# Optimization experiments

Hardware: AMD Instinct MI355X
Metric: run time of the kernel (lower is better)

Reference implementation:

```python
import jax, jax.numpy as jnp
import numpy as np

D_MAIN = 256
D_HID = 512  # int(d_main * d_multiplier)
N_NUM = 96
B = 1024
N_CAND = 100000
LN_EPS = 1e-5


def _ln(x, g, b):
    mu = x.mean(-1, keepdims=True)
    var = ((x - mu) ** 2).mean(-1, keepdims=True)
    return (x - mu) / jnp.sqrt(var + LN_EPS) * g + b


def _block(x, W1, b1, W2, b2):
    # Linear -> ReLU -> (Dropout=id) -> Linear -> (Dropout=id), residual added by caller
    return jnp.maximum(x @ W1 + b1, 0.0) @ W2 + b2


def setup_inputs() -> dict:
    key = jax.random.key(0)
    ks = jax.random.split(key, 32)

    def w(i, shape):
        fan_in = shape[0]
        return jax.random.normal(ks[i], shape, jnp.float32) / np.sqrt(fan_in)

    return {
        "x_num": jax.random.normal(ks[0], (B, N_NUM), jnp.float32),
        "cand_x_num": jax.random.normal(ks[1], (N_CAND, N_NUM), jnp.float32),
        "cand_y": jax.random.normal(ks[2], (N_CAND, 1), jnp.float32),
        "context_size": 96,
        # input linear
        "W_in": w(3, (N_NUM, D_MAIN)), "b_in": jnp.zeros((D_MAIN,), jnp.float32),
        # encoder block (no norm: first block)
        "We1": w(4, (D_MAIN, D_HID)), "be1": jnp.zeros((D_HID,), jnp.float32),
        "We2": w(5, (D_HID, D_MAIN)), "be2": jnp.zeros((D_MAIN,), jnp.float32),
        # mixer LayerNorm (mixer_normalization='auto' with encoder_n_blocks>0)
        "g_m": jnp.ones((D_MAIN,), jnp.float32), "b_m": jnp.zeros((D_MAIN,), jnp.float32),
        # S: key projection
        "Ws": w(6, (D_MAIN, D_MAIN)), "bs": jnp.zeros((D_MAIN,), jnp.float32),
        "Wy": w(7, (1, D_MAIN)), "by": jnp.zeros((D_MAIN,), jnp.float32),
        # V_t: Linear(no bias) -> ReLU -> Linear
        "Wt1": w(8, (D_MAIN, D_HID)),
        "Wt2": w(9, (D_HID, D_MAIN)), "bt2": jnp.zeros((D_MAIN,), jnp.float32),
        # predictor block (no norm: first block)
        "Wp1": w(10, (D_MAIN, D_HID)), "bp1": jnp.zeros((D_HID,), jnp.float32),
        "Wp2": w(11, (D_HID, D_MAIN)), "bp2": jnp.zeros((D_MAIN,), jnp.float32),
        # head P: LayerNorm -> ReLU -> Linear(d_main, 1)
        "g_h": jnp.ones((D_MAIN,), jnp.float32), "b_h": jnp.zeros((D_MAIN,), jnp.float32),
        "Wh": w(12, (D_MAIN, 1)), "bh": jnp.zeros((1,), jnp.float32),
    }


def _encode(x, W_in, b_in, We1, be1, We2, be2, g_m, b_m, Ws, bs):
    h = x @ W_in + b_in
    h = h + _block(h, We1, be1, We2, be2)
    k = _ln(h, g_m, b_m) @ Ws + bs
    return h, k


def reference(x_num, cand_x_num, cand_y, context_size,
              W_in, b_in, We1, be1, We2, be2, g_m, b_m, Ws, bs,
              Wy, by, Wt1, Wt2, bt2, Wp1, bp1, Wp2, bp2, g_h, b_h, Wh, bh):
    # encode queries and candidates with shared weights
    x, k = _encode(x_num, W_in, b_in, We1, be1, We2, be2, g_m, b_m, Ws, bs)
    _, ck = _encode(cand_x_num, W_in, b_in, We1, be1, We2, be2, g_m, b_m, Ws, bs)

    # similarities = -||k - ck||^2  [B, N_CAND]
    sim = (2.0 * (k @ ck.T)
           - (k * k).sum(-1, keepdims=True)
           - (ck * ck).sum(-1)[None, :])

    top_sim, idx = jax.lax.top_k(sim, context_size)   # [B, m]
    probs = jax.nn.softmax(top_sim, axis=-1)           # context_dropout = id in eval

    ctx_k = ck[idx]                                    # [B, m, d_main]
    ctx_y = cand_y[idx]                                # [B, m, 1]

    # values = V_y(y) + V_t(k - ctx_k)
    v = (ctx_y @ Wy + by
         + jnp.maximum((k[:, None, :] - ctx_k) @ Wt1, 0.0) @ Wt2 + bt2)

    x = x + jnp.einsum('bm,bmd->bd', probs, v)

    # predictor block + head
    x = x + _block(x, Wp1, bp1, Wp2, bp2)
    out = jnp.maximum(_ln(x, g_h, b_h), 0.0) @ Wh + bh  # [B, 1]
    return out
```

## Files before the change

### kernel.cpp

```cpp
#include <hip/hip_runtime.h>
#include <stdint.h>

#define NCAND 100000
#define NB    1024
#define DNUM  96
#define DM    256
#define DH    512
#define MCTX  96
#define LNEPS 1e-5f

typedef __bf16 bf16x8 __attribute__((ext_vector_type(8)));
typedef float  f32x4  __attribute__((ext_vector_type(4)));
typedef unsigned short u16x8 __attribute__((ext_vector_type(8)));
typedef unsigned short us;

__device__ __forceinline__ us f2bf(float x)
{
    unsigned u = __float_as_uint(x);
    unsigned r = u + 0x7FFFu + ((u >> 16) & 1u);
    return (us)(r >> 16);
}
__device__ __forceinline__ float bfbits(us h)
{
    return __uint_as_float(((unsigned)h) << 16);
}

extern "C" __global__ __launch_bounds__(256)
void split_k(const float* X, us* Xh, us* Xl, long long n)
{
    long long i = (long long)blockIdx.x * 256 + threadIdx.x;
    if (i < n) {
        float x = X[i];
        us h = f2bf(x);
        Xh[i] = h;
        Xl[i] = f2bf(x - bfbits(h));
    }
}

extern "C" __global__ __launch_bounds__(256)
void packW_k(const float* W, us* Ph, us* Pl, int Kd, int Nd)
{
    int i = blockIdx.x * 256 + threadIdx.x;
    if (i >= Kd * Nd) return;
    int e = i & 7, lane = (i >> 3) & 63, r = i >> 9;
    int KT = Kd >> 5;
    int kt = r % KT, jt = r / KT;
    int n = jt * 16 + (lane & 15);
    int k = kt * 32 + (lane >> 4) * 8 + e;
    float x = W[(long long)k * Nd + n];
    us h = f2bf(x);
    Ph[i] = h;
    Pl[i] = f2bf(x - bfbits(h));
}

extern "C" __global__ __launch_bounds__(256)
void packR_k(const us* Rh, const us* Rl, us* Ph, us* Pl, int Kd, int total)
{
    int i = blockIdx.x * 256 + threadIdx.x;
    if (i >= total) return;
    int e = i & 7, lane = (i >> 3) & 63, r = i >> 9;
    int KT = Kd >> 5;
    int kt = r % KT, jt = r / KT;
    int n = jt * 16 + (lane & 15);
    int k = kt * 32 + (lane >> 4) * 8 + e;
    Ph[i] = Rh[(long long)n * Kd + k];
    Pl[i] = Rl[(long long)n * Kd + k];
}

extern "C" __global__ __launch_bounds__(256)
void gemm_d(const us* Ah, const us* Al, const us* BPh, const us* BPl,
            float* outF, us* outH, us* outL, us* outB16,
            const float* bias, const us* Rh, const us* Rl, int dorelu,
            const float* lng, const float* lnb, us* lnH, us* lnL,
            float* snOut,
            const us* Gqh, const us* Gql, const us* Gch, const us* Gcl,
            const int* gidx,
            float* simT, const float* colb,
            int M, int N, int K)
{
    __shared__ float red1[256];
    __shared__ float red2[256];
    __shared__ float mu_s[64];
    __shared__ float rs_s[64];
    int t = threadIdx.x, wave = t >> 6, lane = t & 63;
    int lm = lane & 15, lk = (lane >> 4) * 8, rb = (lane >> 4) * 4;
    int m0b = blockIdx.x * 64;
    int n0 = blockIdx.y * 256;
    int KT = K >> 5;
    int jt0 = (n0 >> 4) + wave * 4;

    f32x4 acc[4][4];
#pragma unroll
    for (int i = 0; i < 4; i++)
#pragma unroll
        for (int j = 0; j < 4; j++)
            for (int e = 0; e < 4; e++) acc[i][j][e] = 0.0f;

    int gb4[4], gc4[4];
    if (gidx) {
#pragma unroll
        for (int i = 0; i < 4; i++) {
            int grow = m0b + i * 16 + lm;
            if (grow < M) { gb4[i] = grow / MCTX; gc4[i] = gidx[grow]; }
            else          { gb4[i] = 0; gc4[i] = 0; }
        }
    }

    for (int kt = 0; kt < KT; kt++) {
        int k0 = kt * 32;
        bf16x8 fah[4], fal[4];
#pragma unroll
        for (int i = 0; i < 4; i++) {
            int arow = m0b + i * 16 + lm;
            u16x8 ah8 = {0,0,0,0,0,0,0,0}, al8 = ah8;
            if (arow < M) {
                if (!gidx) {
                    ah8 = *(const u16x8*)(Ah + (long long)arow * K + k0 + lk);
                    al8 = *(const u16x8*)(Al + (long long)arow * K + k0 + lk);
                } else {
                    u16x8 qh = *(const u16x8*)(Gqh + (long long)gb4[i] * DM + k0 + lk);
                    u16x8 ql = *(const u16x8*)(Gql + (long long)gb4[i] * DM + k0 + lk);
                    u16x8 ch = *(const u16x8*)(Gch + (long long)gc4[i] * DM + k0 + lk);
                    u16x8 cl = *(const u16x8*)(Gcl + (long long)gc4[i] * DM + k0 + lk);
#pragma unroll
                    for (int e = 0; e < 8; e++) {
                        float v = (bfbits(qh[e]) + bfbits(ql[e]))
                                - (bfbits(ch[e]) + bfbits(cl[e]));
                        ah8[e] = f2bf(v);
                    }
                }
            }
            fah[i] = *(bf16x8*)&ah8;
            fal[i] = *(bf16x8*)&al8;
        }
#pragma unroll
        for (int j = 0; j < 4; j++) {
            long long bo = ((long long)(jt0 + j) * KT + kt) * 512 + lane * 8;
            u16x8 bu  = *(const u16x8*)(BPh + bo);
            u16x8 blu = *(const u16x8*)(BPl + bo);
            bf16x8 fbh = *(bf16x8*)&bu;
            bf16x8 fbl = *(bf16x8*)&blu;
#pragma unroll
            for (int i = 0; i < 4; i++) {
                acc[i][j] = __builtin_amdgcn_mfma_f32_16x16x32_bf16(fah[i], fbh, acc[i][j], 0, 0, 0);
                acc[i][j] = __builtin_amdgcn_mfma_f32_16x16x32_bf16(fah[i], fbl, acc[i][j], 0, 0, 0);
                if (!gidx)
                    acc[i][j] = __builtin_amdgcn_mfma_f32_16x16x32_bf16(fal[i], fbh, acc[i][j], 0, 0, 0);
            }
        }
    }

    if (simT) {
#pragma unroll
        for (int i = 0; i < 4; i++) {
            int cb = m0b + i * 16;
            if (cb >= M) break;
#pragma unroll
            for (int j = 0; j < 4; j++) {
                int q = n0 + wave * 64 + j * 16 + lm;
                f32x4 v;
                for (int e = 0; e < 4; e++)
                    v[e] = 2.0f * acc[i][j][e] - colb[cb + rb + e];
                *(f32x4*)(simT + (long long)q * NCAND + cb + rb) = v;
            }
        }
        return;
    }

#pragma unroll
    for (int j = 0; j < 4; j++) {
        int col = n0 + wave * 64 + j * 16 + lm;
        float bc = bias ? bias[col] : 0.0f;
#pragma unroll
        for (int i = 0; i < 4; i++) {
            for (int e = 0; e < 4; e++) {
                int row = m0b + i * 16 + rb + e;
                float v = acc[i][j][e] + bc;
                if (row < M) {
                    long long oix = (long long)row * N + col;
                    if (Rh) v += bfbits(Rh[oix]) + bfbits(Rl[oix]);
                    if (dorelu && v < 0.0f) v = 0.0f;
                    if (outF)   outF[oix] = v;
                    if (outB16) outB16[oix] = f2bf(v);
                    if (outH) { us h = f2bf(v); outH[oix] = h; outL[oix] = f2bf(v - bfbits(h)); }
                } else {
                    if (dorelu && v < 0.0f) v = 0.0f;
                }
                acc[i][j][e] = v;
            }
        }
    }

    if (lng || snOut) {
#pragma unroll
        for (int i = 0; i < 4; i++) {
            for (int e = 0; e < 4; e++) {
                int lr = i * 16 + rb + e;
                float s1 = 0.0f, s2 = 0.0f;
#pragma unroll
                for (int j = 0; j < 4; j++) { float v = acc[i][j][e]; s1 += v; s2 += v * v; }
                for (int o = 1; o < 16; o <<= 1) {
                    s1 += __shfl_xor(s1, o, 64);
                    s2 += __shfl_xor(s2, o, 64);
                }
                if (lm == 0) { red1[lr * 4 + wave] = s1; red2[lr * 4 + wave] = s2; }
            }
        }
        __syncthreads();
        if (t < 64) {
            float a = red1[t*4] + red1[t*4+1] + red1[t*4+2] + red1[t*4+3];
            float b2 = red2[t*4] + red2[t*4+1] + red2[t*4+2] + red2[t*4+3];
            if (lng) {
                float mu = a * (1.0f / 256.0f);
                float var = b2 * (1.0f / 256.0f) - mu * mu;
                mu_s[t] = mu;
                rs_s[t] = rsqrtf(var + LNEPS);
            }
            if (snOut && (m0b + t) < M) snOut[m0b + t] = b2;
        }
        __syncthreads();
        if (lng) {
#pragma unroll
            for (int j = 0; j < 4; j++) {
                int col = n0 + wave * 64 + j * 16 + lm;
                float g = lng[col], bb = lnb[col];
#pragma unroll
                for (int i = 0; i < 4; i++) {
                    for (int e = 0; e < 4; e++) {
                        int lr = i * 16 + rb + e;
                        int row = m0b + lr;
                        if (row >= M) continue;
                        float y = (acc[i][j][e] - mu_s[lr]) * rs_s[lr] * g + bb;
                        long long oix = (long long)row * N + col;
                        us h = f2bf(y);
                        lnH[oix] = h;
                        lnL[oix] = f2bf(y - bfbits(h));
                    }
                }
            }
        }
    }
}

__device__ unsigned fmapf(float f)
{
    unsigned u = __float_as_uint(f);
    return u ^ (unsigned)(((int)u >> 31) | (int)0x80000000);
}

extern "C" __global__ __launch_bounds__(1024)
void topk_k(const float* S, int q0, int* out_idx, float* out_p)
{
    int t = threadIdx.x;
    const float* row = S + (long long)blockIdx.x * NCAND;
    const float4* row4 = (const float4*)row;
    __shared__ int hist8[8][256];
    __shared__ unsigned sh_prefix;
    __shared__ int sh_want, cntG, cntE;
    __shared__ int   gidx[128];
    __shared__ float gval[128];
    __shared__ int   eqi[2048];
    __shared__ float vals[MCTX];
    __shared__ int   inds[MCTX];
    __shared__ float pr[MCTX];

    if (t == 0) { sh_prefix = 0u; sh_want = MCTX; cntG = 0; cntE = 0; }

    for (int lvl = 0; lvl < 4; lvl++) {
        int shift = 24 - 8 * lvl;
        for (int i = t; i < 2048; i += 1024) ((int*)hist8)[i] = 0;
        __syncthreads();
        unsigned prefix = sh_prefix;
        unsigned mask = (lvl == 0) ? 0u : (0xFFFFFFFFu << (shift + 8));
        int* hrow = hist8[t & 7];
        for (int c = t; c < NCAND / 4; c += 1024) {
            float4 v = row4[c];
            unsigned k0 = fmapf(v.x), k1 = fmapf(v.y), k2 = fmapf(v.z), k3 = fmapf(v.w);
            if ((k0 & mask) == prefix) atomicAdd(&hrow[(k0 >> shift) & 255], 1);
            if ((k1 & mask) == prefix) atomicAdd(&hrow[(k1 >> shift) & 255], 1);
            if ((k2 & mask) == prefix) atomicAdd(&hrow[(k2 >> shift) & 255], 1);
            if ((k3 & mask) == prefix) atomicAdd(&hrow[(k3 >> shift) & 255], 1);
        }
        __syncthreads();
        if (t < 256) {
            int s = 0;
            for (int g2 = 1; g2 < 8; g2++) s += hist8[g2][t];
            hist8[0][t] += s;
        }
        __syncthreads();
        if (t == 0) {
            int want = sh_want, cum = 0;
            for (int b2 = 255; b2 >= 0; b2--) {
                cum += hist8[0][b2];
                if (cum >= want) {
                    sh_want = want - (cum - hist8[0][b2]);
                    sh_prefix = prefix | ((unsigned)b2 << shift);
                    break;
                }
            }
        }
        __syncthreads();
    }
    unsigned T = sh_prefix;
    for (int c = t; c < NCAND / 4; c += 1024) {
        float4 v = row4[c];
        float vv[4]; vv[0] = v.x; vv[1] = v.y; vv[2] = v.z; vv[3] = v.w;
        for (int e = 0; e < 4; e++) {
            unsigned key = fmapf(vv[e]);
            if (key > T) {
                int p = atomicAdd(&cntG, 1);
                if (p < 128) { gidx[p] = c * 4 + e; gval[p] = vv[e]; }
            } else if (key == T) {
                int p = atomicAdd(&cntE, 1);
                if (p < 2048) eqi[p] = c * 4 + e;
            }
        }
    }
    __syncthreads();
    if (t == 0) {
        int nG = cntG; if (nG > MCTX) nG = MCTX;
        int nE = cntE; if (nE > 2048) nE = 2048;
        int need = MCTX - nG;
        for (int i = 0; i < nG; i++) { inds[i] = gidx[i]; vals[i] = gval[i]; }
        for (int s = 0; s < need; s++) {
            int best = 0x7FFFFFFF, bp = -1;
            for (int e = 0; e < nE; e++) if (eqi[e] < best) { best = eqi[e]; bp = e; }
            if (bp >= 0) { eqi[bp] = 0x7FFFFFFF; inds[nG + s] = best; vals[nG + s] = row[best]; }
            else         { inds[nG + s] = 0;     vals[nG + s] = -3.0e38f; }
        }
        float mx = -3.4e38f;
        for (int i = 0; i < MCTX; i++) if (vals[i] > mx) mx = vals[i];
        float sum = 0.0f;
        for (int i = 0; i < MCTX; i++) { float e = expf(vals[i] - mx); pr[i] = e; sum += e; }
        float inv = 1.0f / sum;
        for (int i = 0; i < MCTX; i++) pr[i] *= inv;
    }
    __syncthreads();
    if (t < MCTX) {
        long long o = (long long)(q0 + blockIdx.x) * MCTX + t;
        out_idx[o] = inds[t];
        out_p[o]   = pr[t];
    }
}

extern "C" __global__ __launch_bounds__(256)
void ybar_k(const float* P, const int* idx, const float* y, float* ybar)
{
    __shared__ float sred[256];
    int b = blockIdx.x, t = threadIdx.x;
    float v = 0.0f;
    if (t < MCTX) v = P[(long long)b * MCTX + t] * y[idx[(long long)b * MCTX + t]];
    sred[t] = v; __syncthreads();
    for (int s = 128; s > 0; s >>= 1) { if (t < s) sred[t] += sred[t + s]; __syncthreads(); }
    if (t == 0) ybar[b] = sred[0];
}

extern "C" __global__ __launch_bounds__(512)
void wsum2_k(const float* Pq, const float* R, const float* P, const int* idx, float* u)
{
    __shared__ float pl[MCTX];
    __shared__ int ix[MCTX];
    int b = blockIdx.x, j = threadIdx.x;
    if (j < MCTX) {
        pl[j] = P[(long long)b * MCTX + j];
        ix[j] = idx[(long long)b * MCTX + j];
    }
    __syncthreads();
    float pb = Pq[(long long)b * DH + j];
    float a = 0.0f;
    for (int m = 0; m < MCTX; m++) {
        float d = pb - R[(long long)ix[m] * DH + j];
        a += pl[m] * (d > 0.0f ? d : 0.0f);
    }
    u[(long long)b * DH + j] = a;
}

extern "C" __global__ __launch_bounds__(512)
void wsum_k(const us* U, const float* P, float* u)
{
    __shared__ float pl[MCTX];
    int b = blockIdx.x, j = threadIdx.x;
    if (j < MCTX) pl[j] = P[(long long)b * MCTX + j];
    __syncthreads();
    const us* Ub = U + (long long)b * MCTX * DH;
    float acc = 0.0f;
    for (int m = 0; m < MCTX; m++) acc += pl[m] * bfbits(Ub[(long long)m * DH + j]);
    u[(long long)b * DH + j] = acc;
}

extern "C" __global__ __launch_bounds__(256)
void mixprep_sp(us* h2h, us* h2l, const float* ybar,
                const float* Wy, const float* by, const float* bt2)
{
    int b = blockIdx.x, d = threadIdx.x;
    long long i = (long long)b * DM + d;
    float v = bfbits(h2h[i]) + bfbits(h2l[i]) + ybar[b] * Wy[d] + by[d] + bt2[d];
    us h = f2bf(v);
    h2h[i] = h;
    h2l[i] = f2bf(v - bfbits(h));
}

extern "C" __global__ __launch_bounds__(256)
void head_k(const float* X, const float* g, const float* bln, const float* Wh,
            const float* bh, float* out)
{
    __shared__ float sred[256];
    int r = blockIdx.x, t = threadIdx.x;
    float x = X[(long long)r * DM + t];
    sred[t] = x; __syncthreads();
    for (int s = 128; s > 0; s >>= 1) { if (t < s) sred[t] += sred[t + s]; __syncthreads(); }
    float mu = sred[0] * (1.0f / DM); __syncthreads();
    float d = x - mu;
    sred[t] = d * d; __syncthreads();
    for (int s = 128; s > 0; s >>= 1) { if (t < s) sred[t] += sred[t + s]; __syncthreads(); }
    float var = sred[0] * (1.0f / DM); __syncthreads();
    float ln = d * rsqrtf(var + LNEPS) * g[t] + bln[t];
    float rl = (ln > 0.0f) ? ln : 0.0f;
    sred[t] = rl * Wh[t]; __syncthreads();
    for (int s = 128; s > 0; s >>= 1) { if (t < s) sred[t] += sred[t + s]; __syncthreads(); }
    if (t == 0) out[r] = sred[0] + bh[0];
}

#define ZU (us*)0
#define ZCU (const us*)0
#define ZF (float*)0
#define ZCF (const float*)0
#define ZI (const int*)0

extern "C" void kernel_launch(void* const* d_in, const int* in_sizes, int n_in,
                              void* d_out, int out_size, void* d_ws, size_t ws_size,
                              hipStream_t stream)
{
    const float* x_num  = (const float*)d_in[0];
    const float* cand_x = (const float*)d_in[1];
    const float* cand_y = (const float*)d_in[2];
    const float* W_in = (const float*)d_in[4];
    const float* b_in = (const float*)d_in[5];
    const float* We1  = (const float*)d_in[6];
    const float* be1  = (const float*)d_in[7];
    const float* We2  = (const float*)d_in[8];
    const float* be2  = (const float*)d_in[9];
    const float* g_m  = (const float*)d_in[10];
    const float* b_m  = (const float*)d_in[11];
    const float* Ws   = (const float*)d_in[12];
    const float* bs   = (const float*)d_in[13];
    const float* Wy   = (const float*)d_in[14];
    const float* by   = (const float*)d_in[15];
    const float* Wt1  = (const float*)d_in[16];
    const float* Wt2  = (const float*)d_in[17];
    const float* bt2  = (const float*)d_in[18];
    const float* Wp1  = (const float*)d_in[19];
    const float* bp1  = (const float*)d_in[20];
    const float* Wp2  = (const float*)d_in[21];
    const float* bp2  = (const float*)d_in[22];
    const float* g_h  = (const float*)d_in[23];
    const float* b_h  = (const float*)d_in[24];
    const float* Wh   = (const float*)d_in[25];
    const float* bh   = (const float*)d_in[26];
    float* out = (float*)d_out;

    char* p = (char*)d_ws;
    us* WinPh = (us*)p; p += 256*96*2;   us* WinPl = (us*)p; p += 256*96*2;
    us* We1Ph = (us*)p; p += 512*256*2;  us* We1Pl = (us*)p; p += 512*256*2;
    us* We2Ph = (us*)p; p += 256*512*2;  us* We2Pl = (us*)p; p += 256*512*2;
    us* WsPh  = (us*)p; p += 256*256*2;  us* WsPl  = (us*)p; p += 256*256*2;
    us* Wt1Ph = (us*)p; p += 512*256*2;  us* Wt1Pl = (us*)p; p += 512*256*2;
    us* Wt2Ph = (us*)p; p += 256*512*2;  us* Wt2Pl = (us*)p; p += 256*512*2;
    us* Wp1Ph = (us*)p; p += 512*256*2;  us* Wp1Pl = (us*)p; p += 512*256*2;
    us* Wp2Ph = (us*)p; p += 256*512*2;  us* Wp2Pl = (us*)p; p += 256*512*2;
    us* XNh  = (us*)p; p += (long long)NB*DNUM*2;  us* XNl  = (us*)p; p += (long long)NB*DNUM*2;
    us* HQ1h = (us*)p; p += (long long)NB*DM*2;    us* HQ1l = (us*)p; p += (long long)NB*DM*2;
    us* TQh  = (us*)p; p += (long long)NB*DH*2;    us* TQl  = (us*)p; p += (long long)NB*DH*2;
    us* HQ2h = (us*)p; p += (long long)NB*DM*2;    us* HQ2l = (us*)p; p += (long long)NB*DM*2;
    us* LNQh = (us*)p; p += (long long)NB*DM*2;    us* LNQl = (us*)p; p += (long long)NB*DM*2;
    us* KQh  = (us*)p; p += (long long)NB*DM*2;    us* KQl  = (us*)p; p += (long long)NB*DM*2;
    us* KQPh = (us*)p; p += (long long)NB*DM*2;    us* KQPl = (us*)p; p += (long long)NB*DM*2;
    us* XQh  = (us*)p; p += (long long)NB*DM*2;    us* XQl  = (us*)p; p += (long long)NB*DM*2;
    us* UQvh = (us*)p; p += (long long)NB*DH*2;    us* UQvl = (us*)p; p += (long long)NB*DH*2;
    float* UQv  = (float*)p; p += (long long)NB*DH*4;
    float* Pq   = (float*)p; p += (long long)NB*DH*4;
    float* XQ2f = (float*)p; p += (long long)NB*DM*4;
    float* YB   = (float*)p; p += (long long)NB*4;
    int*   IDX  = (int*)p;   p += (long long)NB*MCTX*4;
    float* PRB  = (float*)p; p += (long long)NB*MCTX*4;
    us* KCh = (us*)p; p += (long long)NCAND*DM*2;  us* KCl = (us*)p; p += (long long)NCAND*DM*2;
    float* SC = (float*)p; p += (long long)NCAND*4;

    size_t used = (size_t)(p - (char*)d_ws);
    long long avail = (ws_size > used + 4096) ? (long long)(ws_size - used - 4096) : 0;
    int EC = 6250;
    if      (avail >= 243300000LL) EC = 50000;
    else if (avail >= 141000000LL) EC = 25000;
    else if (avail >=  89700000LL) EC = 12500;
    int QS = (avail >= 204800000LL) ? 512 : 256;
    int tierA = (avail >= 204800000LL) ? 1 : 0;
    int VC = (avail >= 100700000LL) ? 1024 : 512;

    char* AR = p;
    us* CXh = (us*)AR;
    us* CXl = CXh + (long long)NCAND*DNUM;
    char* EB = AR + (long long)NCAND*DNUM*4;
    us* Hch  = (us*)EB;                              us* Hcl  = Hch + (long long)EC*DM;
    us* Tch  = (us*)(EB + (long long)EC*DM*4);       us* Tcl  = Tch + (long long)EC*DH;
    us* LNch = (us*)(EB + (long long)EC*(DM+DH)*4);  us* LNcl = LNch + (long long)EC*DM;
    float* Sb = (float*)AR;
    float* R  = (float*)AR;
    us* Ub = (us*)AR;

    dim3 blk(256);

    packW_k<<<dim3((DNUM*DM+255)/256), blk, 0, stream>>>(W_in, WinPh, WinPl, DNUM, DM);
    packW_k<<<dim3((DM*DH+255)/256), blk, 0, stream>>>(We1, We1Ph, We1Pl, DM, DH);
    packW_k<<<dim3((DH*DM+255)/256), blk, 0, stream>>>(We2, We2Ph, We2Pl, DH, DM);
    packW_k<<<dim3((DM*DM+255)/256), blk, 0, stream>>>(Ws,  WsPh,  WsPl,  DM, DM);
    packW_k<<<dim3((DM*DH+255)/256), blk, 0, stream>>>(Wt1, Wt1Ph, Wt1Pl, DM, DH);
    packW_k<<<dim3((DH*DM+255)/256), blk, 0, stream>>>(Wt2, Wt2Ph, Wt2Pl, DH, DM);
    packW_k<<<dim3((DM*DH+255)/256), blk, 0, stream>>>(Wp1, Wp1Ph, Wp1Pl, DM, DH);
    packW_k<<<dim3((DH*DM+255)/256), blk, 0, stream>>>(Wp2, Wp2Ph, Wp2Pl, DH, DM);
    split_k<<<dim3((NB*DNUM+255)/256), blk, 0, stream>>>(x_num, XNh, XNl, (long long)NB*DNUM);
    split_k<<<dim3((NCAND*DNUM+255)/256), blk, 0, stream>>>(cand_x, CXh, CXl, (long long)NCAND*DNUM);

    gemm_d<<<dim3(NB/64, 1), blk, 0, stream>>>(XNh, XNl, WinPh, WinPl,
        ZF, HQ1h, HQ1l, ZU, b_in, ZCU, ZCU, 0, ZCF, ZCF, ZU, ZU, ZF,
        ZCU, ZCU, ZCU, ZCU, ZI, ZF, ZCF, NB, DM, DNUM);
    gemm_d<<<dim3(NB/64, 2), blk, 0, stream>>>(HQ1h, HQ1l, We1Ph, We1Pl,
        ZF, TQh, TQl, ZU, be1, ZCU, ZCU, 1, ZCF, ZCF, ZU, ZU, ZF,
        ZCU, ZCU, ZCU, ZCU, ZI, ZF, ZCF, NB, DH, DM);
    gemm_d<<<dim3(NB/64, 1), blk, 0, stream>>>(TQh, TQl, We2Ph, We2Pl,
        ZF, HQ2h, HQ2l, ZU, be2, HQ1h, HQ1l, 0, g_m, b_m, LNQh, LNQl, ZF,
        ZCU, ZCU, ZCU, ZCU, ZI, ZF, ZCF, NB, DM, DH);
    gemm_d<<<dim3(NB/64, 1), blk, 0, stream>>>(LNQh, LNQl, WsPh, WsPl,
        ZF, KQh, KQl, ZU, bs, ZCU, ZCU, 0, ZCF, ZCF, ZU, ZU, ZF,
        ZCU, ZCU, ZCU, ZCU, ZI, ZF, ZCF, NB, DM, DM);
    packR_k<<<dim3((NB*DM+255)/256), blk, 0, stream>>>(KQh, KQl, KQPh, KQPl, DM, NB*DM);

    for (int c0 = 0; c0 < NCAND; c0 += EC) {
        int gx = (EC + 63) / 64;
        gemm_d<<<dim3(gx, 1), blk, 0, stream>>>(CXh + (long long)c0*DNUM, CXl + (long long)c0*DNUM,
            WinPh, WinPl, ZF, Hch, Hcl, ZU, b_in, ZCU, ZCU, 0, ZCF, ZCF, ZU, ZU, ZF,
            ZCU, ZCU, ZCU, ZCU, ZI, ZF, ZCF, EC, DM, DNUM);
        gemm_d<<<dim3(gx, 2), blk, 0, stream>>>(Hch, Hcl, We1Ph, We1Pl,
            ZF, Tch, Tcl, ZU, be1, ZCU, ZCU, 1, ZCF, ZCF, ZU, ZU, ZF,
            ZCU, ZCU, ZCU, ZCU, ZI, ZF, ZCF, EC, DH, DM);
        gemm_d<<<dim3(gx, 1), blk, 0, stream>>>(Tch, Tcl, We2Ph, We2Pl,
            ZF, ZU, ZU, ZU, be2, Hch, Hcl, 0, g_m, b_m, LNch, LNcl, ZF,
            ZCU, ZCU, ZCU, ZCU, ZI, ZF, ZCF, EC, DM, DH);
        gemm_d<<<dim3(gx, 1), blk, 0, stream>>>(LNch, LNcl, WsPh, WsPl,
            ZF, KCh + (long long)c0*DM, KCl + (long long)c0*DM, ZU, bs, ZCU, ZCU, 0,
            ZCF, ZCF, ZU, ZU, SC + c0,
            ZCU, ZCU, ZCU, ZCU, ZI, ZF, ZCF, EC, DM, DM);
    }

    for (int q0 = 0; q0 < NB; q0 += QS) {
        gemm_d<<<dim3((NCAND + 63) / 64, QS / 256), blk, 0, stream>>>(KCh, KCl,
            KQPh + (long long)q0*DM, KQPl + (long long)q0*DM,
            ZF, ZU, ZU, ZU, ZCF, ZCU, ZCU, 0, ZCF, ZCF, ZU, ZU, ZF,
            ZCU, ZCU, ZCU, ZCU, ZI, Sb, SC, NCAND, QS, DM);
        topk_k<<<dim3(QS), dim3(1024), 0, stream>>>(Sb, q0, IDX, PRB);
    }

    ybar_k<<<dim3(NB), blk, 0, stream>>>(PRB, IDX, cand_y, YB);
    gemm_d<<<dim3(NB/64, 2), blk, 0, stream>>>(KQh, KQl, Wt1Ph, Wt1Pl,
        Pq, ZU, ZU, ZU, ZCF, ZCU, ZCU, 0, ZCF, ZCF, ZU, ZU, ZF,
        ZCU, ZCU, ZCU, ZCU, ZI, ZF, ZCF, NB, DH, DM);
    if (tierA) {
        gemm_d<<<dim3((NCAND + 63) / 64, 2), blk, 0, stream>>>(KCh, KCl, Wt1Ph, Wt1Pl,
            R, ZU, ZU, ZU, ZCF, ZCU, ZCU, 0, ZCF, ZCF, ZU, ZU, ZF,
            ZCU, ZCU, ZCU, ZCU, ZI, ZF, ZCF, NCAND, DH, DM);
        wsum2_k<<<dim3(NB), dim3(512), 0, stream>>>(Pq, R, PRB, IDX, UQv);
    } else {
        for (int v0 = 0; v0 < NB; v0 += VC) {
            gemm_d<<<dim3((VC * MCTX) / 64, 2), blk, 0, stream>>>(ZCU, ZCU, Wt1Ph, Wt1Pl,
                ZF, ZU, ZU, Ub, ZCF, ZCU, ZCU, 1, ZCF, ZCF, ZU, ZU, ZF,
                KQh + (long long)v0*DM, KQl + (long long)v0*DM, KCh, KCl,
                IDX + (long long)v0*MCTX, ZF, ZCF, VC * MCTX, DH, DM);
            wsum_k<<<dim3(VC), dim3(512), 0, stream>>>(Ub, PRB + (long long)v0*MCTX,
                                                       UQv + (long long)v0*DH);
        }
    }
    split_k<<<dim3((NB*DH+255)/256), blk, 0, stream>>>(UQv, UQvh, UQvl, (long long)NB*DH);
    mixprep_sp<<<dim3(NB), blk, 0, stream>>>(HQ2h, HQ2l, YB, Wy, by, bt2);
    gemm_d<<<dim3(NB/64, 1), blk, 0, stream>>>(UQvh, UQvl, Wt2Ph, Wt2Pl,
        ZF, XQh, XQl, ZU, ZCF, HQ2h, HQ2l, 0, ZCF, ZCF, ZU, ZU, ZF,
        ZCU, ZCU, ZCU, ZCU, ZI, ZF, ZCF, NB, DM, DH);

    gemm_d<<<dim3(NB/64, 2), blk, 0, stream>>>(XQh, XQl, Wp1Ph, Wp1Pl,
        ZF, TQh, TQl, ZU, bp1, ZCU, ZCU, 1, ZCF, ZCF, ZU, ZU, ZF,
        ZCU, ZCU, ZCU, ZCU, ZI, ZF, ZCF, NB, DH, DM);
    gemm_d<<<dim3(NB/64, 1), blk, 0, stream>>>(TQh, TQl, Wp2Ph, Wp2Pl,
        XQ2f, ZU, ZU, ZU, bp2, XQh, XQl, 0, ZCF, ZCF, ZU, ZU, ZF,
        ZCU, ZCU, ZCU, ZCU, ZI, ZF, ZCF, NB, DM, DH);
    head_k<<<dim3(NB), blk, 0, stream>>>(XQ2f, g_h, b_h, Wh, bh, out);
}
```

Baseline: 3.463 ms.

## Pre-pack key matrices into MFMA fragment layout for coalesced A-operand loads

Result: slower. 3.719 ms (+7.4%).

```diff
diff --git a/kernel.cpp b/kernel.cpp
--- a/kernel.cpp
+++ b/kernel.cpp
@@ -68,6 +68,22 @@
 }
 
 extern "C" __global__ __launch_bounds__(256)
+void packA_k(const us* Sh, const us* Sl, us* Ph, us* Pl, int Kd, long long total)
+{
+    long long i = (long long)blockIdx.x * 256 + threadIdx.x;
+    if (i >= total) return;
+    int e = (int)(i & 7), lane = (int)((i >> 3) & 63);
+    long long r = i >> 9;
+    int KT = Kd >> 5;
+    int kt = (int)(r % KT);
+    long long mt = r / KT;
+    long long m = mt * 16 + (lane & 15);
+    int k = kt * 32 + (lane >> 4) * 8 + e;
+    Ph[i] = Sh[m * Kd + k];
+    Pl[i] = Sl[m * Kd + k];
+}
+
+extern "C" __global__ __launch_bounds__(256)
 void gemm_d(const us* Ah, const us* Al, const us* BPh, const us* BPl,
             float* outF, us* outH, us* outL, us* outB16,
             const float* bias, const us* Rh, const us* Rl, int dorelu,
@@ -76,7 +92,7 @@
             const us* Gqh, const us* Gql, const us* Gch, const us* Gcl,
             const int* gidx,
             float* simT, const float* colb,
-            int M, int N, int K)
+            int M, int N, int K, int apk)
 {
     __shared__ float red1[256];
     __shared__ float red2[256];
@@ -96,38 +112,52 @@
         for (int j = 0; j < 4; j++)
             for (int e = 0; e < 4; e++) acc[i][j][e] = 0.0f;
 
-    int gb4[4], gc4[4];
+    long long qb4[4], cb4[4];
     if (gidx) {
 #pragma unroll
         for (int i = 0; i < 4; i++) {
             int grow = m0b + i * 16 + lm;
-            if (grow < M) { gb4[i] = grow / MCTX; gc4[i] = gidx[grow]; }
-            else          { gb4[i] = 0; gc4[i] = 0; }
-        }
-    }
+            int gq = 0, gc = 0;
+            if (grow < M) { gq = grow / MCTX; gc = gidx[grow]; }
+            qb4[i] = (((long long)(gq >> 4) * 8) * 64 + (gq & 15) + (lane >> 4) * 16) * 8;
+            cb4[i] = (((long long)(gc >> 4) * 8) * 64 + (gc & 15) + (lane >> 4) * 16) * 8;
+        }
+    }
+    int MT = M >> 4;
 
     for (int kt = 0; kt < KT; kt++) {
         int k0 = kt * 32;
         bf16x8 fah[4], fal[4];
 #pragma unroll
         for (int i = 0; i < 4; i++) {
-            int arow = m0b + i * 16 + lm;
             u16x8 ah8 = {0,0,0,0,0,0,0,0}, al8 = ah8;
-            if (arow < M) {
-                if (!gidx) {
-                    ah8 = *(const u16x8*)(Ah + (long long)arow * K + k0 + lk);
-                    al8 = *(const u16x8*)(Al + (long long)arow * K + k0 + lk);
+            if (!gidx) {
+                if (!apk) {
+                    int arow = m0b + i * 16 + lm;
+                    if (arow < M) {
+                        ah8 = *(const u16x8*)(Ah + (long long)arow * K + k0 + lk);
+                        al8 = *(const u16x8*)(Al + (long long)arow * K + k0 + lk);
+                    }
                 } else {
-                    u16x8 qh = *(const u16x8*)(Gqh + (long long)gb4[i] * DM + k0 + lk);
-                    u16x8 ql = *(const u16x8*)(Gql + (long long)gb4[i] * DM + k0 + lk);
-                    u16x8 ch = *(const u16x8*)(Gch + (long long)gc4[i] * DM + k0 + lk);
-                    u16x8 cl = *(const u16x8*)(Gcl + (long long)gc4[i] * DM + k0 + lk);
-#pragma unroll
-                    for (int e = 0; e < 8; e++) {
-                        float v = (bfbits(qh[e]) + bfbits(ql[e]))
-                                - (bfbits(ch[e]) + bfbits(cl[e]));
-                        ah8[e] = f2bf(v);
+                    int mt = (m0b >> 4) + i;
+                    if (mt < MT) {
+                        long long bo = ((long long)mt * KT + kt) * 512 + lane * 8;
+                        ah8 = *(const u16x8*)(Ah + bo);
+                        al8 = *(const u16x8*)(Al + bo);
                     }
+                }
+            } else {
+                long long qo = qb4[i] + (long long)kt * 512;
+                long long co = cb4[i] + (long long)kt * 512;
+                u16x8 qh = *(const u16x8*)(Gqh + qo);
+                u16x8 ql = *(const u16x8*)(Gql + qo);
+                u16x8 ch = *(const u16x8*)(Gch + co);
+                u16x8 cl = *(const u16x8*)(Gcl + co);
+#pragma unroll
+                for (int e = 0; e < 8; e++) {
+                    float v = (bfbits(qh[e]) + bfbits(ql[e]))
+                            - (bfbits(ch[e]) + bfbits(cl[e]));
+                    ah8[e] = f2bf(v);
                 }
             }
             fah[i] = *(bf16x8*)&ah8;
@@ -475,6 +505,7 @@
     us* LNQh = (us*)p; p += (long long)NB*DM*2;    us* LNQl = (us*)p; p += (long long)NB*DM*2;
     us* KQh  = (us*)p; p += (long long)NB*DM*2;    us* KQl  = (us*)p; p += (long long)NB*DM*2;
     us* KQPh = (us*)p; p += (long long)NB*DM*2;    us* KQPl = (us*)p; p += (long long)NB*DM*2;
+    us* KQAh = (us*)p; p += (long long)NB*DM*2;    us* KQAl = (us*)p; p += (long long)NB*DM*2;
     us* XQh  = (us*)p; p += (long long)NB*DM*2;    us* XQl  = (us*)p; p += (long long)NB*DM*2;
     us* UQvh = (us*)p; p += (long long)NB*DH*2;    us* UQvl = (us*)p; p += (long long)NB*DH*2;
     float* UQv  = (float*)p; p += (long long)NB*DH*4;
@@ -483,15 +514,15 @@
     float* YB   = (float*)p; p += (long long)NB*4;
     int*   IDX  = (int*)p;   p += (long long)NB*MCTX*4;
     float* PRB  = (float*)p; p += (long long)NB*MCTX*4;
-    us* KCh = (us*)p; p += (long long)NCAND*DM*2;  us* KCl = (us*)p; p += (long long)NCAND*DM*2;
+    us* KCAh = (us*)p; p += (long long)NCAND*DM*2;  us* KCAl = (us*)p; p += (long long)NCAND*DM*2;
     float* SC = (float*)p; p += (long long)NCAND*4;
 
     size_t used = (size_t)(p - (char*)d_ws);
     long long avail = (ws_size > used + 4096) ? (long long)(ws_size - used - 4096) : 0;
-    int EC = 6250;
-    if      (avail >= 243300000LL) EC = 50000;
-    else if (avail >= 141000000LL) EC = 25000;
-    else if (avail >=  89700000LL) EC = 12500;
+    int EC = 6400;
+    if      (avail >= 301000000LL) EC = 51200;
+    else if (avail >= 170000000LL) EC = 25600;
+    else if (avail >= 104500000LL) EC = 12800;
     int QS = (avail >= 204800000LL) ? 512 : 256;
     int tierA = (avail >= 204800000LL) ? 1 : 0;
     int VC = (avail >= 100700000LL) ? 1024 : 512;
@@ -500,9 +531,10 @@
     us* CXh = (us*)AR;
     us* CXl = CXh + (long long)NCAND*DNUM;
     char* EB = AR + (long long)NCAND*DNUM*4;
-    us* Hch  = (us*)EB;                              us* Hcl  = Hch + (long long)EC*DM;
-    us* Tch  = (us*)(EB + (long long)EC*DM*4);       us* Tcl  = Tch + (long long)EC*DH;
-    us* LNch = (us*)(EB + (long long)EC*(DM+DH)*4);  us* LNcl = LNch + (long long)EC*DM;
+    us* Hch  = (us*)EB;                               us* Hcl  = Hch + (long long)EC*DM;
+    us* Tch  = (us*)(EB + (long long)EC*DM*4);        us* Tcl  = Tch + (long long)EC*DH;
+    us* LNch = (us*)(EB + (long long)EC*(DM+DH)*4);   us* LNcl = LNch + (long long)EC*DM;
+    us* KCrh = (us*)(EB + (long long)EC*(2*DM+DH)*4); us* KCrl = KCrh + (long long)EC*DM;
     float* Sb = (float*)AR;
     float* R  = (float*)AR;
     us* Ub = (us*)AR;
@@ -522,58 +554,62 @@
 
     gemm_d<<<dim3(NB/64, 1), blk, 0, stream>>>(XNh, XNl, WinPh, WinPl,
         ZF, HQ1h, HQ1l, ZU, b_in, ZCU, ZCU, 0, ZCF, ZCF, ZU, ZU, ZF,
-        ZCU, ZCU, ZCU, ZCU, ZI, ZF, ZCF, NB, DM, DNUM);
+        ZCU, ZCU, ZCU, ZCU, ZI, ZF, ZCF, NB, DM, DNUM, 0);
     gemm_d<<<dim3(NB/64, 2), blk, 0, stream>>>(HQ1h, HQ1l, We1Ph, We1Pl,
         ZF, TQh, TQl, ZU, be1, ZCU, ZCU, 1, ZCF, ZCF, ZU, ZU, ZF,
-        ZCU, ZCU, ZCU, ZCU, ZI, ZF, ZCF, NB, DH, DM);
+        ZCU, ZCU, ZCU, ZCU, ZI, ZF, ZCF, NB, DH, DM, 0);
     gemm_d<<<dim3(NB/64, 1), blk, 0, stream>>>(TQh, TQl, We2Ph, We2Pl,
         ZF, HQ2h, HQ2l, ZU, be2, HQ1h, HQ1l, 0, g_m, b_m, LNQh, LNQl, ZF,
-        ZCU, ZCU, ZCU, ZCU, ZI, ZF, ZCF, NB, DM, DH);
+        ZCU, ZCU, ZCU, ZCU, ZI, ZF, ZCF, NB, DM, DH, 0);
     gemm_d<<<dim3(NB/64, 1), blk, 0, stream>>>(LNQh, LNQl, WsPh, WsPl,
         ZF, KQh, KQl, ZU, bs, ZCU, ZCU, 0, ZCF, ZCF, ZU, ZU, ZF,
-        ZCU, ZCU, ZCU, ZCU, ZI, ZF, ZCF, NB, DM, DM);
+        ZCU, ZCU, ZCU, ZCU, ZI, ZF, ZCF, NB, DM, DM, 0);
     packR_k<<<dim3((NB*DM+255)/256), blk, 0, stream>>>(KQh, KQl, KQPh, KQPl, DM, NB*DM);
+    packA_k<<<dim3((NB*DM+255)/256), blk, 0, stream>>>(KQh, KQl, KQAh, KQAl, DM, (long long)NB*DM);
 
     for (int c0 = 0; c0 < NCAND; c0 += EC) {
-        int gx = (EC + 63) / 64;
+        int Mc = (NCAND - c0 < EC) ? (NCAND - c0) : EC;
+        int gx = (Mc + 63) / 64;
         gemm_d<<<dim3(gx, 1), blk, 0, stream>>>(CXh + (long long)c0*DNUM, CXl + (long long)c0*DNUM,
             WinPh, WinPl, ZF, Hch, Hcl, ZU, b_in, ZCU, ZCU, 0, ZCF, ZCF, ZU, ZU, ZF,
-            ZCU, ZCU, ZCU, ZCU, ZI, ZF, ZCF, EC, DM, DNUM);
+            ZCU, ZCU, ZCU, ZCU, ZI, ZF, ZCF, Mc, DM, DNUM, 0);
         gemm_d<<<dim3(gx, 2), blk, 0, stream>>>(Hch, Hcl, We1Ph, We1Pl,
             ZF, Tch, Tcl, ZU, be1, ZCU, ZCU, 1, ZCF, ZCF, ZU, ZU, ZF,
-            ZCU, ZCU, ZCU, ZCU, ZI, ZF, ZCF, EC, DH, DM);
+            ZCU, ZCU, ZCU, ZCU, ZI, ZF, ZCF, Mc, DH, DM, 0);
         gemm_d<<<dim3(gx, 1), blk, 0, stream>>>(Tch, Tcl, We2Ph, We2Pl,
             ZF, ZU, ZU, ZU, be2, Hch, Hcl, 0, g_m, b_m, LNch, LNcl, ZF,
-            ZCU, ZCU, ZCU, ZCU, ZI, ZF, ZCF, EC, DM, DH);
+            ZCU, ZCU, ZCU, ZCU, ZI, ZF, ZCF, Mc, DM, DH, 0);
         gemm_d<<<dim3(gx, 1), blk, 0, stream>>>(LNch, LNcl, WsPh, WsPl,
-            ZF, KCh + (long long)c0*DM, KCl + (long long)c0*DM, ZU, bs, ZCU, ZCU, 0,
+            ZF, KCrh, KCrl, ZU, bs, ZCU, ZCU, 0,
             ZCF, ZCF, ZU, ZU, SC + c0,
-            ZCU, ZCU, ZCU, ZCU, ZI, ZF, ZCF, EC, DM, DM);
+            ZCU, ZCU, ZCU, ZCU, ZI, ZF, ZCF, Mc, DM, DM, 0);
+        packA_k<<<dim3((int)(((long long)Mc*DM + 255) / 256)), blk, 0, stream>>>(
+            KCrh, KCrl, KCAh + (long long)c0*DM, KCAl + (long long)c0*DM, DM, (long long)Mc*DM);
     }
 
     for (int q0 = 0; q0 < NB; q0 += QS) {
-        gemm_d<<<dim3((NCAND + 63) / 64, QS / 256), blk, 0, stream>>>(KCh, KCl,
+        gemm_d<<<dim3((NCAND + 63) / 64, QS / 256), blk, 0, stream>>>(KCAh, KCAl,
             KQPh + (long long)q0*DM, KQPl + (long long)q0*DM,
             ZF, ZU, ZU, ZU, ZCF, ZCU, ZCU, 0, ZCF, ZCF, ZU, ZU, ZF,
-            ZCU, ZCU, ZCU, ZCU, ZI, Sb, SC, NCAND, QS, DM);
+            ZCU, ZCU, ZCU, ZCU, ZI, Sb, SC, NCAND, QS, DM, 1);
         topk_k<<<dim3(QS), dim3(1024), 0, stream>>>(Sb, q0, IDX, PRB);
     }
 
     ybar_k<<<dim3(NB), blk, 0, stream>>>(PRB, IDX, cand_y, YB);
-    gemm_d<<<dim3(NB/64, 2), blk, 0, stream>>>(KQh, KQl, Wt1Ph, Wt1Pl,
+    gemm_d<<<dim3(NB/64, 2), blk, 0, stream>>>(KQAh, KQAl, Wt1Ph, Wt1Pl,
         Pq, ZU, ZU, ZU, ZCF, ZCU, ZCU, 0, ZCF, ZCF, ZU, ZU, ZF,
-        ZCU, ZCU, ZCU, ZCU, ZI, ZF, ZCF, NB, DH, DM);
+        ZCU, ZCU, ZCU, ZCU, ZI, ZF, ZCF, NB, DH, DM, 1);
     if (tierA) {
-        gemm_d<<<dim3((NCAND + 63) / 64, 2), blk, 0, stream>>>(KCh, KCl, Wt1Ph, Wt1Pl,
+        gemm_d<<<dim3((NCAND + 63) / 64, 2), blk, 0, stream>>>(KCAh, KCAl, Wt1Ph, Wt1Pl,
             R, ZU, ZU, ZU, ZCF, ZCU, ZCU, 0, ZCF, ZCF, ZU, ZU, ZF,
-            ZCU, ZCU, ZCU, ZCU, ZI, ZF, ZCF, NCAND, DH, DM);
+            ZCU, ZCU, ZCU, ZCU, ZI, ZF, ZCF, NCAND, DH, DM, 1);
         wsum2_k<<<dim3(NB), dim3(512), 0, stream>>>(Pq, R, PRB, IDX, UQv);
     } else {
         for (int v0 = 0; v0 < NB; v0 += VC) {
             gemm_d<<<dim3((VC * MCTX) / 64, 2), blk, 0, stream>>>(ZCU, ZCU, Wt1Ph, Wt1Pl,
                 ZF, ZU, ZU, Ub, ZCF, ZCU, ZCU, 1, ZCF, ZCF, ZU, ZU, ZF,
-                KQh + (long long)v0*DM, KQl + (long long)v0*DM, KCh, KCl,
-                IDX + (long long)v0*MCTX, ZF, ZCF, VC * MCTX, DH, DM);
+                KQAh + (long long)((v0/MCTX>0)?0:0), KQAl, KCAh, KCAl,
+                IDX + (long long)v0*MCTX, ZF, ZCF, VC * MCTX, DH, DM, 0);
             wsum_k<<<dim3(VC), dim3(512), 0, stream>>>(Ub, PRB + (long long)v0*MCTX,
                                                        UQv + (long long)v0*DH);
         }
@@ -582,13 +618,13 @@
     mixprep_sp<<<dim3(NB), blk, 0, stream>>>(HQ2h, HQ2l, YB, Wy, by, bt2);
     gemm_d<<<dim3(NB/64, 1), blk, 0, stream>>>(UQvh, UQvl, Wt2Ph, Wt2Pl,
         ZF, XQh, XQl, ZU, ZCF, HQ2h, HQ2l, 0, ZCF, ZCF, ZU, ZU, ZF,
-        ZCU, ZCU, ZCU, ZCU, ZI, ZF, ZCF, NB, DM, DH);
+        ZCU, ZCU, ZCU, ZCU, ZI, ZF, ZCF, NB, DM, DH, 0);
 
     gemm_d<<<dim3(NB/64, 2), blk, 0, stream>>>(XQh, XQl, Wp1Ph, Wp1Pl,
         ZF, TQh, TQl, ZU, bp1, ZCU, ZCU, 1, ZCF, ZCF, ZU, ZU, ZF,
-        ZCU, ZCU, ZCU, ZCU, ZI, ZF, ZCF, NB, DH, DM);
+        ZCU, ZCU, ZCU, ZCU, ZI, ZF, ZCF, NB, DH, DM, 0);
     gemm_d<<<dim3(NB/64, 1), blk, 0, stream>>>(TQh, TQl, Wp2Ph, Wp2Pl,
         XQ2f, ZU, ZU, ZU, bp2, XQh, XQl, 0, ZCF, ZCF, ZU, ZU, ZF,
-        ZCU, ZCU, ZCU, ZCU, ZI, ZF, ZCF, NB, DM, DH);
+        ZCU, ZCU, ZCU, ZCU, ZI, ZF, ZCF, NB, DM, DH, 0);
     head_k<<<dim3(NB), blk, 0, stream>>>(XQ2f, g_h, b_h, Wh, bh, out);
 }
```
